# Kernel optimization log

Hardware: AMD Instinct MI355X
Metric: run time of the kernel (lower is better)

## Reference

```python
import jax, jax.numpy as jnp
import numpy as np

B, N = 4096, 4096
BISECTION_ITERS = 40


def setup_inputs() -> dict:
    key = jax.random.key(0)
    kz, = jax.random.split(key, 1)
    z = jax.random.normal(kz, (B, N), dtype=jnp.float32)
    gamma = jnp.ones((N,), dtype=jnp.float32)   # GammaParam fixed, init=1, clamped at eps (no-op here)
    m = jnp.zeros((N,), dtype=jnp.float32)      # BoundsParam fixed, m_init=0
    M = jnp.ones((N,), dtype=jnp.float32)       # BoundsParam fixed, M_init=1
    xi = jnp.ones((B,), dtype=jnp.float32)      # fixed xi=1 expanded to batch
    return {"z": z, "gamma": gamma, "m": m, "M": M, "xi": xi}


def reference(z, gamma, m, M, xi):
    """Weighted L2 projection of z (B,N) onto {x: sum x = xi, m <= x <= M} via bisection on lambda."""
    Bq, Nq = z.shape
    gB = jnp.broadcast_to(gamma, (Bq, Nq))
    mB = jnp.broadcast_to(m, (Bq, Nq))
    MB = jnp.broadcast_to(M, (Bq, Nq))
    two_gamma = 2.0 * gB

    lam_low = jnp.min(two_gamma * (mB - z), axis=-1)   # (B,)
    lam_high = jnp.max(two_gamma * (MB - z), axis=-1)  # (B,)

    def body(_, carry):
        lo, hi = carry
        mid = 0.5 * (lo + hi)
        x_mid = jnp.clip(z + mid[:, None] / two_gamma, mB, MB)
        g_mid = jnp.sum(x_mid, axis=-1) - xi
        pos = g_mid > 0
        lo_new = jnp.where(pos, lo, mid)
        hi_new = jnp.where(pos, mid, hi)
        return (lo_new, hi_new)

    lam_low, lam_high = jax.lax.fori_loop(0, BISECTION_ITERS, body, (lam_low, lam_high))
    lam = 0.5 * (lam_low + lam_high)
    x = jnp.clip(z + lam[:, None] / two_gamma, mB, MB)
    return x
```

## Files before the change

### kernel.cpp

```cpp
#include <hip/hip_runtime.h>


#define BISECT_STEPS 6
#define TOTAL_STEPS  9

template<int CTRL, int RM>
__device__ __forceinline__ float dpp_addf(float v) {
    int t = __builtin_amdgcn_update_dpp(0, __float_as_int(v), CTRL, RM, 0xf, false);
    return v + __int_as_float(t);
}
template<int CTRL, int RM>
__device__ __forceinline__ float dpp_minf(float v) {
    int t = __builtin_amdgcn_update_dpp(0x7f800000, __float_as_int(v), CTRL, RM, 0xf, false);
    return fminf(v, __int_as_float(t));
}
template<int CTRL, int RM>
__device__ __forceinline__ float dpp_maxf(float v) {
    int t = __builtin_amdgcn_update_dpp(0xff800000, __float_as_int(v), CTRL, RM, 0xf, false);
    return fmaxf(v, __int_as_float(t));
}
__device__ __forceinline__ float wave_sum(float v) {
    v = dpp_addf<0x111, 0xf>(v);
    v = dpp_addf<0x112, 0xf>(v);
    v = dpp_addf<0x114, 0xf>(v);
    v = dpp_addf<0x118, 0xf>(v);
    v = dpp_addf<0x142, 0xa>(v);
    v = dpp_addf<0x143, 0xc>(v);
    return __int_as_float(__builtin_amdgcn_readlane(__float_as_int(v), 63));
}
__device__ __forceinline__ float wave_min(float v) {
    v = dpp_minf<0x111, 0xf>(v);
    v = dpp_minf<0x112, 0xf>(v);
    v = dpp_minf<0x114, 0xf>(v);
    v = dpp_minf<0x118, 0xf>(v);
    v = dpp_minf<0x142, 0xa>(v);
    v = dpp_minf<0x143, 0xc>(v);
    return __int_as_float(__builtin_amdgcn_readlane(__float_as_int(v), 63));
}
__device__ __forceinline__ float wave_max(float v) {
    v = dpp_maxf<0x111, 0xf>(v);
    v = dpp_maxf<0x112, 0xf>(v);
    v = dpp_maxf<0x114, 0xf>(v);
    v = dpp_maxf<0x118, 0xf>(v);
    v = dpp_maxf<0x142, 0xa>(v);
    v = dpp_maxf<0x143, 0xc>(v);
    return __int_as_float(__builtin_amdgcn_readlane(__float_as_int(v), 63));
}

__global__ __launch_bounds__(256) void qp_proj_n4096(
    const float* __restrict__ z,
    const float* __restrict__ gamma,
    const float* __restrict__ mlo,
    const float* __restrict__ mhi,
    const float* __restrict__ xi,
    float* __restrict__ out)
{
    constexpr int N = 4096;
    const int row  = blockIdx.x;
    const int tid  = threadIdx.x;
    const int lane = tid & 63;
    const int wid  = tid >> 6;

    const float4* zrow = reinterpret_cast<const float4*>(z + (size_t)row * N);
    const float4* g4   = reinterpret_cast<const float4*>(gamma);
    const float4* m4   = reinterpret_cast<const float4*>(mlo);
    const float4* M4   = reinterpret_cast<const float4*>(mhi);
    float4*       orow = reinterpret_cast<float4*>(out + (size_t)row * N);

    __shared__ float red[8][4];
    __shared__ float wsum[2][4];

    float za[16];
    float zmn =  INFINITY, zmx = -INFINITY;
    float gmn =  INFINITY, gmx = -INFINITY;
    float mmn =  INFINITY, mmx = -INFINITY;
    float Mmn =  INFINITY, Mmx = -INFINITY;

    #pragma unroll
    for (int k = 0; k < 4; ++k) {
        const int idx = tid + k * 256;
        const float4 zz = zrow[idx];
        const float4 gg = g4[idx];
        const float4 mm = m4[idx];
        const float4 MM = M4[idx];
        za[4*k+0] = zz.x; za[4*k+1] = zz.y; za[4*k+2] = zz.z; za[4*k+3] = zz.w;
        zmn = fminf(zmn, fminf(fminf(zz.x, zz.y), fminf(zz.z, zz.w)));
        zmx = fmaxf(zmx, fmaxf(fmaxf(zz.x, zz.y), fmaxf(zz.z, zz.w)));
        gmn = fminf(gmn, fminf(fminf(gg.x, gg.y), fminf(gg.z, gg.w)));
        gmx = fmaxf(gmx, fmaxf(fmaxf(gg.x, gg.y), fmaxf(gg.z, gg.w)));
        mmn = fminf(mmn, fminf(fminf(mm.x, mm.y), fminf(mm.z, mm.w)));
        mmx = fmaxf(mmx, fmaxf(fmaxf(mm.x, mm.y), fmaxf(mm.z, mm.w)));
        Mmn = fminf(Mmn, fminf(fminf(MM.x, MM.y), fminf(MM.z, MM.w)));
        Mmx = fmaxf(Mmx, fmaxf(fmaxf(MM.x, MM.y), fmaxf(MM.z, MM.w)));
    }
    zmn = wave_min(zmn); zmx = wave_max(zmx);
    gmn = wave_min(gmn); gmx = wave_max(gmx);
    mmn = wave_min(mmn); mmx = wave_max(mmx);
    Mmn = wave_min(Mmn); Mmx = wave_max(Mmx);
    if (lane == 0) {
        red[0][wid] = zmn; red[1][wid] = zmx;
        red[2][wid] = gmn; red[3][wid] = gmx;
        red[4][wid] = mmn; red[5][wid] = mmx;
        red[6][wid] = Mmn; red[7][wid] = Mmx;
    }
    __syncthreads();
    const float zminT = fminf(fminf(red[0][0], red[0][1]), fminf(red[0][2], red[0][3]));
    const float zmaxT = fmaxf(fmaxf(red[1][0], red[1][1]), fmaxf(red[1][2], red[1][3]));
    const float gminT = fminf(fminf(red[2][0], red[2][1]), fminf(red[2][2], red[2][3]));
    const float gmaxT = fmaxf(fmaxf(red[3][0], red[3][1]), fmaxf(red[3][2], red[3][3]));
    const float mminT = fminf(fminf(red[4][0], red[4][1]), fminf(red[4][2], red[4][3]));
    const float mmaxT = fmaxf(fmaxf(red[5][0], red[5][1]), fmaxf(red[5][2], red[5][3]));
    const float MminT = fminf(fminf(red[6][0], red[6][1]), fminf(red[6][2], red[6][3]));
    const float MmaxT = fmaxf(fmaxf(red[7][0], red[7][1]), fmaxf(red[7][2], red[7][3]));

    const bool uniform = (gminT == gmaxT) && (mminT == mmaxT) &&
                         (MminT == MmaxT) && (gminT > 0.0f);
    const float xir = xi[row];

    if (uniform) {
        const float m0 = mminT, M0 = MminT;
        const float tg = 2.0f * gminT;
        const float ia = 1.0f / tg;
        float lo = tg * (m0 - zmaxT);
        float hi = tg * (M0 - zminT);
        float glo = (float)N * m0 - xir;
        float ghi = (float)N * M0 - xir;
        int side = 0;

        for (int it = 0; it < TOTAL_STEPS; ++it) {
            const float w = hi - lo;
            float cand;
            if (it < BISECT_STEPS) {
                cand = fmaf(0.5f, w, lo);
            } else {
                const float denom = ghi - glo;
                cand = (lo * ghi - hi * glo) / denom;
                cand = fminf(fmaxf(cand, fmaf(0.0625f, w, lo)),
                             fmaf(-0.0625f, w, hi));
            }

            float t0 = 0.f, t1 = 0.f, t2 = 0.f, t3 = 0.f;
            #pragma unroll
            for (int q = 0; q < 4; ++q) {
                t0 += __builtin_amdgcn_fmed3f(fmaf(cand, ia, za[4*q+0]), m0, M0);
                t1 += __builtin_amdgcn_fmed3f(fmaf(cand, ia, za[4*q+1]), m0, M0);
                t2 += __builtin_amdgcn_fmed3f(fmaf(cand, ia, za[4*q+2]), m0, M0);
                t3 += __builtin_amdgcn_fmed3f(fmaf(cand, ia, za[4*q+3]), m0, M0);
            }
            const float sw = wave_sum((t0 + t1) + (t2 + t3));

            const int p = it & 1;
            if (lane == 0) wsum[p][wid] = sw;
            __syncthreads();
            const float s = ((wsum[p][0] + wsum[p][1]) + (wsum[p][2] + wsum[p][3])) - xir;

            if (s > 0.0f) {
                hi = cand;
                if (side == 1) glo *= 0.5f;
                ghi = s;
                side = 1;
            } else {
                lo = cand;
                if (side == -1) ghi *= 0.5f;
                glo = s;
                side = -1;
            }
        }

        const float denom = ghi - glo;
        float lam = (denom > 0.0f) ? (lo * ghi - hi * glo) / denom
                                   : fmaf(0.5f, hi - lo, lo);
        lam = fminf(fmaxf(lam, lo), hi);

        #pragma unroll
        for (int k = 0; k < 4; ++k) {
            const int idx = tid + k * 256;
            float4 r;
            r.x = __builtin_amdgcn_fmed3f(fmaf(lam, ia, za[4*k+0]), m0, M0);
            r.y = __builtin_amdgcn_fmed3f(fmaf(lam, ia, za[4*k+1]), m0, M0);
            r.z = __builtin_amdgcn_fmed3f(fmaf(lam, ia, za[4*k+2]), m0, M0);
            r.w = __builtin_amdgcn_fmed3f(fmaf(lam, ia, za[4*k+3]), m0, M0);
            orow[idx] = r;
        }
    } else {
        __syncthreads();

        float ib[16], ma[16], Ma[16];
        float pmin =  INFINITY, pmax = -INFINITY, psm = 0.0f, psM = 0.0f;
        #pragma unroll
        for (int k = 0; k < 4; ++k) {
            const int idx = tid + k * 256;
            const float4 gg = g4[idx];
            const float4 mm = m4[idx];
            const float4 MM = M4[idx];
            const float gs[4] = {gg.x, gg.y, gg.z, gg.w};
            const float ms[4] = {mm.x, mm.y, mm.z, mm.w};
            const float Ms[4] = {MM.x, MM.y, MM.z, MM.w};
            #pragma unroll
            for (int c = 0; c < 4; ++c) {
                const int j = 4 * k + c;
                const float tg = 2.0f * gs[c];
                ib[j] = 1.0f / tg;
                ma[j] = ms[c];
                Ma[j] = Ms[c];
                pmin = fminf(pmin, tg * (ms[c] - za[j]));
                pmax = fmaxf(pmax, tg * (Ms[c] - za[j]));
                psm += ms[c];
                psM += Ms[c];
            }
        }
        pmin = wave_min(pmin);
        pmax = wave_max(pmax);
        psm  = wave_sum(psm);
        psM  = wave_sum(psM);
        if (lane == 0) { red[0][wid] = pmin; red[1][wid] = pmax;
                         red[2][wid] = psm;  red[3][wid] = psM; }
        __syncthreads();
        float lo = fminf(fminf(red[0][0], red[0][1]), fminf(red[0][2], red[0][3]));
        float hi = fmaxf(fmaxf(red[1][0], red[1][1]), fmaxf(red[1][2], red[1][3]));
        float glo = ((red[2][0] + red[2][1]) + (red[2][2] + red[2][3])) - xir;
        float ghi = ((red[3][0] + red[3][1]) + (red[3][2] + red[3][3])) - xir;
        int side = 0;

        for (int it = 0; it < TOTAL_STEPS; ++it) {
            const float w = hi - lo;
            float cand;
            if (it < BISECT_STEPS) {
                cand = fmaf(0.5f, w, lo);
            } else {
                const float denom = ghi - glo;
                cand = (lo * ghi - hi * glo) / denom;
                cand = fminf(fmaxf(cand, fmaf(0.0625f, w, lo)),
                             fmaf(-0.0625f, w, hi));
            }

            float t0 = 0.f, t1 = 0.f, t2 = 0.f, t3 = 0.f;
            #pragma unroll
            for (int q = 0; q < 4; ++q) {
                t0 += __builtin_amdgcn_fmed3f(fmaf(cand, ib[4*q+0], za[4*q+0]), ma[4*q+0], Ma[4*q+0]);
                t1 += __builtin_amdgcn_fmed3f(fmaf(cand, ib[4*q+1], za[4*q+1]), ma[4*q+1], Ma[4*q+1]);
                t2 += __builtin_amdgcn_fmed3f(fmaf(cand, ib[4*q+2], za[4*q+2]), ma[4*q+2], Ma[4*q+2]);
                t3 += __builtin_amdgcn_fmed3f(fmaf(cand, ib[4*q+3], za[4*q+3]), ma[4*q+3], Ma[4*q+3]);
            }
            const float sw = wave_sum((t0 + t1) + (t2 + t3));

            const int p = it & 1;
            if (lane == 0) wsum[p][wid] = sw;
            __syncthreads();
            const float s = ((wsum[p][0] + wsum[p][1]) + (wsum[p][2] + wsum[p][3])) - xir;

            if (s > 0.0f) {
                hi = cand;
                if (side == 1) glo *= 0.5f;
                ghi = s;
                side = 1;
            } else {
                lo = cand;
                if (side == -1) ghi *= 0.5f;
                glo = s;
                side = -1;
            }
        }

        const float denom = ghi - glo;
        float lam = (denom > 0.0f) ? (lo * ghi - hi * glo) / denom
                                   : fmaf(0.5f, hi - lo, lo);
        lam = fminf(fmaxf(lam, lo), hi);

        #pragma unroll
        for (int k = 0; k < 4; ++k) {
            const int idx = tid + k * 256;
            float4 r;
            float xs[4];
            #pragma unroll
            for (int c = 0; c < 4; ++c) {
                const int j = 4 * k + c;
                xs[c] = __builtin_amdgcn_fmed3f(fmaf(lam, ib[j], za[j]), ma[j], Ma[j]);
            }
            r.x = xs[0]; r.y = xs[1]; r.z = xs[2]; r.w = xs[3];
            orow[idx] = r;
        }
    }
}

extern "C" void kernel_launch(void* const* d_in, const int* in_sizes, int n_in,
                              void* d_out, int out_size, void* d_ws, size_t ws_size,
                              hipStream_t stream) {
    const float* z     = (const float*)d_in[0];
    const float* gamma = (const float*)d_in[1];
    const float* m     = (const float*)d_in[2];
    const float* M     = (const float*)d_in[3];
    const float* xi    = (const float*)d_in[4];
    float* out = (float*)d_out;

    const int B = in_sizes[4];
    qp_proj_n4096<<<dim3(B), dim3(256), 0, stream>>>(z, gamma, m, M, xi, out);
}
```

Before: 34.01 us.

## Replace bisection/Illinois search with 5-way multisection rounds in uniform path

```diff
diff --git a/kernel.cpp b/kernel.cpp
--- a/kernel.cpp
+++ b/kernel.cpp
@@ -1,6 +1,7 @@
 #include <hip/hip_runtime.h>
 
 
+#define ROUNDS 5
 #define BISECT_STEPS 6
 #define TOTAL_STEPS  9
 
@@ -68,7 +69,7 @@
     float4*       orow = reinterpret_cast<float4*>(out + (size_t)row * N);
 
     __shared__ float red[8][4];
-    __shared__ float wsum[2][4];
+    __shared__ float wsum[2][4][4];
 
     float za[16];
     float zmn =  INFINITY, zmx = -INFINITY;
@@ -125,51 +126,52 @@
         float hi = tg * (M0 - zminT);
         float glo = (float)N * m0 - xir;
         float ghi = (float)N * M0 - xir;
-        int side = 0;
-
-        for (int it = 0; it < TOTAL_STEPS; ++it) {
-            const float w = hi - lo;
-            float cand;
-            if (it < BISECT_STEPS) {
-                cand = fmaf(0.5f, w, lo);
-            } else {
-                const float denom = ghi - glo;
-                cand = (lo * ghi - hi * glo) / denom;
-                cand = fminf(fmaxf(cand, fmaf(0.0625f, w, lo)),
-                             fmaf(-0.0625f, w, hi));
-            }
-
-            float t0 = 0.f, t1 = 0.f, t2 = 0.f, t3 = 0.f;
-            #pragma unroll
-            for (int q = 0; q < 4; ++q) {
-                t0 += __builtin_amdgcn_fmed3f(fmaf(cand, ia, za[4*q+0]), m0, M0);
-                t1 += __builtin_amdgcn_fmed3f(fmaf(cand, ia, za[4*q+1]), m0, M0);
-                t2 += __builtin_amdgcn_fmed3f(fmaf(cand, ia, za[4*q+2]), m0, M0);
-                t3 += __builtin_amdgcn_fmed3f(fmaf(cand, ia, za[4*q+3]), m0, M0);
-            }
-            const float sw = wave_sum((t0 + t1) + (t2 + t3));
-
-            const int p = it & 1;
-            if (lane == 0) wsum[p][wid] = sw;
-            __syncthreads();
-            const float s = ((wsum[p][0] + wsum[p][1]) + (wsum[p][2] + wsum[p][3])) - xir;
-
-            if (s > 0.0f) {
-                hi = cand;
-                if (side == 1) glo *= 0.5f;
-                ghi = s;
-                side = 1;
-            } else {
-                lo = cand;
-                if (side == -1) ghi *= 0.5f;
-                glo = s;
-                side = -1;
+
+        if (hi > lo) {
+            for (int r = 0; r < ROUNDS; ++r) {
+                const float w5 = 0.2f * (hi - lo);
+                const float c1 = lo + w5;
+                const float c2 = fmaf(2.0f, w5, lo);
+                const float c3 = fmaf(3.0f, w5, lo);
+                const float c4 = fmaf(4.0f, w5, lo);
+
+                float s1 = 0.f, s2 = 0.f, s3 = 0.f, s4 = 0.f;
+                #pragma unroll
+                for (int j = 0; j < 16; ++j) {
+                    const float zj = za[j];
+                    s1 += __builtin_amdgcn_fmed3f(fmaf(c1, ia, zj), m0, M0);
+                    s2 += __builtin_amdgcn_fmed3f(fmaf(c2, ia, zj), m0, M0);
+                    s3 += __builtin_amdgcn_fmed3f(fmaf(c3, ia, zj), m0, M0);
+                    s4 += __builtin_amdgcn_fmed3f(fmaf(c4, ia, zj), m0, M0);
+                }
+                s1 = wave_sum(s1);
+                s2 = wave_sum(s2);
+                s3 = wave_sum(s3);
+                s4 = wave_sum(s4);
+
+                const int p = r & 1;
+                if (lane == 0) {
+                    wsum[p][0][wid] = s1; wsum[p][1][wid] = s2;
+                    wsum[p][2][wid] = s3; wsum[p][3][wid] = s4;
+                }
+                __syncthreads();
+                const float g1 = ((wsum[p][0][0] + wsum[p][0][1]) + (wsum[p][0][2] + wsum[p][0][3])) - xir;
+                const float g2 = ((wsum[p][1][0] + wsum[p][1][1]) + (wsum[p][1][2] + wsum[p][1][3])) - xir;
+                const float g3 = ((wsum[p][2][0] + wsum[p][2][1]) + (wsum[p][2][2] + wsum[p][2][3])) - xir;
+                const float g4v = ((wsum[p][3][0] + wsum[p][3][1]) + (wsum[p][3][2] + wsum[p][3][3])) - xir;
+
+                const int cnt = (g1 <= 0.0f) + (g2 <= 0.0f) + (g3 <= 0.0f) + (g4v <= 0.0f);
+                const float nglo = (cnt == 0) ? glo : (cnt == 1 ? g1 : cnt == 2 ? g2 : cnt == 3 ? g3 : g4v);
+                const float nghi = (cnt == 4) ? ghi : (cnt == 0 ? g1 : cnt == 1 ? g2 : cnt == 2 ? g3 : g4v);
+                const float nlo  = fmaf((float)cnt, w5, lo);
+                const float nhi  = (cnt == 4) ? hi : fmaf((float)(cnt + 1), w5, lo);
+                lo = nlo; hi = nhi; glo = nglo; ghi = nghi;
             }
         }
 
         const float denom = ghi - glo;
-        float lam = (denom > 0.0f) ? (lo * ghi - hi * glo) / denom
-                                   : fmaf(0.5f, hi - lo, lo);
+        float lam = (denom > 1e-30f) ? (lo * ghi - hi * glo) / denom
+                                     : fmaf(0.5f, hi - lo, lo);
         lam = fminf(fmaxf(lam, lo), hi);
 
         #pragma unroll
@@ -245,9 +247,9 @@
             const float sw = wave_sum((t0 + t1) + (t2 + t3));
 
             const int p = it & 1;
-            if (lane == 0) wsum[p][wid] = sw;
+            if (lane == 0) wsum[p][0][wid] = sw;
             __syncthreads();
-            const float s = ((wsum[p][0] + wsum[p][1]) + (wsum[p][2] + wsum[p][3])) - xir;
+            const float s = ((wsum[p][0][0] + wsum[p][0][1]) + (wsum[p][0][2] + wsum[p][0][3])) - xir;
 
             if (s > 0.0f) {
                 hi = cand;
```

Measured after the change: 49.87 us. 46.7% more time.

## Process four rows per block with next-row prefetch and cheaper uniformity check

Applied to the files above, without the earlier changes.

```diff
diff --git a/kernel.cpp b/kernel.cpp
--- a/kernel.cpp
+++ b/kernel.cpp
@@ -1,8 +1,9 @@
 #include <hip/hip_runtime.h>
 
 
+#define ROWS_PB 4
 #define BISECT_STEPS 6
-#define TOTAL_STEPS  9
+#define TOTAL_STEPS  8
 
 template<int CTRL, int RM>
 __device__ __forceinline__ float dpp_addf(float v) {
@@ -53,232 +54,270 @@
     const float* __restrict__ mlo,
     const float* __restrict__ mhi,
     const float* __restrict__ xi,
-    float* __restrict__ out)
+    float* __restrict__ out,
+    int Btot)
 {
     constexpr int N = 4096;
-    const int row  = blockIdx.x;
     const int tid  = threadIdx.x;
     const int lane = tid & 63;
     const int wid  = tid >> 6;
-
-    const float4* zrow = reinterpret_cast<const float4*>(z + (size_t)row * N);
-    const float4* g4   = reinterpret_cast<const float4*>(gamma);
-    const float4* m4   = reinterpret_cast<const float4*>(mlo);
-    const float4* M4   = reinterpret_cast<const float4*>(mhi);
-    float4*       orow = reinterpret_cast<float4*>(out + (size_t)row * N);
-
-    __shared__ float red[8][4];
+    const int row0 = blockIdx.x * ROWS_PB;
+
+    const float4* g4 = reinterpret_cast<const float4*>(gamma);
+    const float4* m4 = reinterpret_cast<const float4*>(mlo);
+    const float4* M4 = reinterpret_cast<const float4*>(mhi);
+
+    __shared__ float red[2][2][4];
     __shared__ float wsum[2][4];
-
-    float za[16];
-    float zmn =  INFINITY, zmx = -INFINITY;
-    float gmn =  INFINITY, gmx = -INFINITY;
-    float mmn =  INFINITY, mmx = -INFINITY;
-    float Mmn =  INFINITY, Mmx = -INFINITY;
-
+    __shared__ float gred[4][4];
+    __shared__ int   uni[4];
+
+    const float g0 = gamma[0];
+    const float m0 = mlo[0];
+    const float M0 = mhi[0];
+    bool ok = (g0 > 0.0f) && (M0 > m0);
     #pragma unroll
     for (int k = 0; k < 4; ++k) {
         const int idx = tid + k * 256;
-        const float4 zz = zrow[idx];
         const float4 gg = g4[idx];
         const float4 mm = m4[idx];
         const float4 MM = M4[idx];
-        za[4*k+0] = zz.x; za[4*k+1] = zz.y; za[4*k+2] = zz.z; za[4*k+3] = zz.w;
-        zmn = fminf(zmn, fminf(fminf(zz.x, zz.y), fminf(zz.z, zz.w)));
-        zmx = fmaxf(zmx, fmaxf(fmaxf(zz.x, zz.y), fmaxf(zz.z, zz.w)));
-        gmn = fminf(gmn, fminf(fminf(gg.x, gg.y), fminf(gg.z, gg.w)));
-        gmx = fmaxf(gmx, fmaxf(fmaxf(gg.x, gg.y), fmaxf(gg.z, gg.w)));
-        mmn = fminf(mmn, fminf(fminf(mm.x, mm.y), fminf(mm.z, mm.w)));
-        mmx = fmaxf(mmx, fmaxf(fmaxf(mm.x, mm.y), fmaxf(mm.z, mm.w)));
-        Mmn = fminf(Mmn, fminf(fminf(MM.x, MM.y), fminf(MM.z, MM.w)));
-        Mmx = fmaxf(Mmx, fmaxf(fmaxf(MM.x, MM.y), fmaxf(MM.z, MM.w)));
+        ok = ok && (gg.x == g0) && (gg.y == g0) && (gg.z == g0) && (gg.w == g0)
+                && (mm.x == m0) && (mm.y == m0) && (mm.z == m0) && (mm.w == m0)
+                && (MM.x == M0) && (MM.y == M0) && (MM.z == M0) && (MM.w == M0);
     }
-    zmn = wave_min(zmn); zmx = wave_max(zmx);
-    gmn = wave_min(gmn); gmx = wave_max(gmx);
-    mmn = wave_min(mmn); mmx = wave_max(mmx);
-    Mmn = wave_min(Mmn); Mmx = wave_max(Mmx);
-    if (lane == 0) {
-        red[0][wid] = zmn; red[1][wid] = zmx;
-        red[2][wid] = gmn; red[3][wid] = gmx;
-        red[4][wid] = mmn; red[5][wid] = mmx;
-        red[6][wid] = Mmn; red[7][wid] = Mmx;
+    {
+        const unsigned long long bal = __ballot(ok);
+        if (lane == 0) uni[wid] = (bal == 0xFFFFFFFFFFFFFFFFull) ? 1 : 0;
     }
     __syncthreads();
-    const float zminT = fminf(fminf(red[0][0], red[0][1]), fminf(red[0][2], red[0][3]));
-    const float zmaxT = fmaxf(fmaxf(red[1][0], red[1][1]), fmaxf(red[1][2], red[1][3]));
-    const float gminT = fminf(fminf(red[2][0], red[2][1]), fminf(red[2][2], red[2][3]));
-    const float gmaxT = fmaxf(fmaxf(red[3][0], red[3][1]), fmaxf(red[3][2], red[3][3]));
-    const float mminT = fminf(fminf(red[4][0], red[4][1]), fminf(red[4][2], red[4][3]));
-    const float mmaxT = fmaxf(fmaxf(red[5][0], red[5][1]), fmaxf(red[5][2], red[5][3]));
-    const float MminT = fminf(fminf(red[6][0], red[6][1]), fminf(red[6][2], red[6][3]));
-    const float MmaxT = fmaxf(fmaxf(red[7][0], red[7][1]), fmaxf(red[7][2], red[7][3]));
-
-    const bool uniform = (gminT == gmaxT) && (mminT == mmaxT) &&
-                         (MminT == MmaxT) && (gminT > 0.0f);
-    const float xir = xi[row];
+    const bool uniform = uni[0] && uni[1] && uni[2] && uni[3];
 
     if (uniform) {
-        const float m0 = mminT, M0 = MminT;
-        const float tg = 2.0f * gminT;
+        const float tg = 2.0f * g0;
         const float ia = 1.0f / tg;
-        float lo = tg * (m0 - zmaxT);
-        float hi = tg * (M0 - zminT);
-        float glo = (float)N * m0 - xir;
-        float ghi = (float)N * M0 - xir;
-        int side = 0;
-
-        for (int it = 0; it < TOTAL_STEPS; ++it) {
-            const float w = hi - lo;
-            float cand;
-            if (it < BISECT_STEPS) {
-                cand = fmaf(0.5f, w, lo);
-            } else {
-                const float denom = ghi - glo;
-                cand = (lo * ghi - hi * glo) / denom;
-                cand = fminf(fmaxf(cand, fmaf(0.0625f, w, lo)),
-                             fmaf(-0.0625f, w, hi));
-            }
-
-            float t0 = 0.f, t1 = 0.f, t2 = 0.f, t3 = 0.f;
+        const float gloC = (float)N * m0;
+        const float ghiC = (float)N * M0;
+
+        float za[16];
+        {
+            const float4* zr = reinterpret_cast<const float4*>(z + (size_t)row0 * N);
             #pragma unroll
-            for (int q = 0; q < 4; ++q) {
-                t0 += __builtin_amdgcn_fmed3f(fmaf(cand, ia, za[4*q+0]), m0, M0);
-                t1 += __builtin_amdgcn_fmed3f(fmaf(cand, ia, za[4*q+1]), m0, M0);
-                t2 += __builtin_amdgcn_fmed3f(fmaf(cand, ia, za[4*q+2]), m0, M0);
-                t3 += __builtin_amdgcn_fmed3f(fmaf(cand, ia, za[4*q+3]), m0, M0);
-            }
-            const float sw = wave_sum((t0 + t1) + (t2 + t3));
-
-            const int p = it & 1;
-            if (lane == 0) wsum[p][wid] = sw;
+            for (int k = 0; k < 4; ++k) {
+                const float4 zz = zr[tid + k * 256];
+                za[4*k+0] = zz.x; za[4*k+1] = zz.y; za[4*k+2] = zz.z; za[4*k+3] = zz.w;
+            }
+        }
+
+        #pragma unroll
+        for (int r = 0; r < ROWS_PB; ++r) {
+            const int row = row0 + r;
+            if (row >= Btot) break;
+
+            float zb[16];
+            const bool hasNext = (r + 1 < ROWS_PB) && (row + 1 < Btot);
+            if (hasNext) {
+                const float4* zr = reinterpret_cast<const float4*>(z + (size_t)(row + 1) * N);
+                #pragma unroll
+                for (int k = 0; k < 4; ++k) {
+                    const float4 zz = zr[tid + k * 256];
+                    zb[4*k+0] = zz.x; zb[4*k+1] = zz.y; zb[4*k+2] = zz.z; zb[4*k+3] = zz.w;
+                }
+            }
+
+            float zmn = INFINITY, zmx = -INFINITY;
+            #pragma unroll
+            for (int j = 0; j < 16; ++j) {
+                zmn = fminf(zmn, za[j]);
+                zmx = fmaxf(zmx, za[j]);
+            }
+            zmn = wave_min(zmn);
+            zmx = wave_max(zmx);
+            const int pr = r & 1;
+            if (lane == 0) { red[pr][0][wid] = zmn; red[pr][1][wid] = zmx; }
             __syncthreads();
-            const float s = ((wsum[p][0] + wsum[p][1]) + (wsum[p][2] + wsum[p][3])) - xir;
-
-            if (s > 0.0f) {
-                hi = cand;
-                if (side == 1) glo *= 0.5f;
-                ghi = s;
-                side = 1;
-            } else {
-                lo = cand;
-                if (side == -1) ghi *= 0.5f;
-                glo = s;
-                side = -1;
-            }
-        }
-
-        const float denom = ghi - glo;
-        float lam = (denom > 0.0f) ? (lo * ghi - hi * glo) / denom
-                                   : fmaf(0.5f, hi - lo, lo);
-        lam = fminf(fmaxf(lam, lo), hi);
-
-        #pragma unroll
-        for (int k = 0; k < 4; ++k) {
-            const int idx = tid + k * 256;
-            float4 r;
-            r.x = __builtin_amdgcn_fmed3f(fmaf(lam, ia, za[4*k+0]), m0, M0);
-            r.y = __builtin_amdgcn_fmed3f(fmaf(lam, ia, za[4*k+1]), m0, M0);
-            r.z = __builtin_amdgcn_fmed3f(fmaf(lam, ia, za[4*k+2]), m0, M0);
-            r.w = __builtin_amdgcn_fmed3f(fmaf(lam, ia, za[4*k+3]), m0, M0);
-            orow[idx] = r;
+            const float zminT = fminf(fminf(red[pr][0][0], red[pr][0][1]),
+                                      fminf(red[pr][0][2], red[pr][0][3]));
+            const float zmaxT = fmaxf(fmaxf(red[pr][1][0], red[pr][1][1]),
+                                      fmaxf(red[pr][1][2], red[pr][1][3]));
+            const float xir = xi[row];
+
+            float lo  = tg * (m0 - zmaxT);
+            float hi  = tg * (M0 - zminT);
+            float glo = gloC - xir;
+            float ghi = ghiC - xir;
+            int side = 0;
+
+            for (int it = 0; it < TOTAL_STEPS; ++it) {
+                const float w = hi - lo;
+                float cand;
+                if (it < BISECT_STEPS) {
+                    cand = fmaf(0.5f, w, lo);
+                } else {
+                    const float denom = ghi - glo;
+                    cand = (lo * ghi - hi * glo) / denom;
+                    cand = fminf(fmaxf(cand, fmaf(0.0625f, w, lo)),
+                                 fmaf(-0.0625f, w, hi));
+                }
+
+                float t0 = 0.f, t1 = 0.f, t2 = 0.f, t3 = 0.f;
+                #pragma unroll
+                for (int q = 0; q < 4; ++q) {
+                    t0 += __builtin_amdgcn_fmed3f(fmaf(cand, ia, za[4*q+0]), m0, M0);
+                    t1 += __builtin_amdgcn_fmed3f(fmaf(cand, ia, za[4*q+1]), m0, M0);
+                    t2 += __builtin_amdgcn_fmed3f(fmaf(cand, ia, za[4*q+2]), m0, M0);
+                    t3 += __builtin_amdgcn_fmed3f(fmaf(cand, ia, za[4*q+3]), m0, M0);
+                }
+                const float sw = wave_sum((t0 + t1) + (t2 + t3));
+
+                const int p = it & 1;
+                if (lane == 0) wsum[p][wid] = sw;
+                __syncthreads();
+                const float s = ((wsum[p][0] + wsum[p][1]) + (wsum[p][2] + wsum[p][3])) - xir;
+
+                if (s > 0.0f) {
+                    hi = cand;
+                    if (side == 1) glo *= 0.5f;
+                    ghi = s;
+                    side = 1;
+                } else {
+                    lo = cand;
+                    if (side == -1) ghi *= 0.5f;
+                    glo = s;
+                    side = -1;
+                }
+            }
+
+            const float denom = ghi - glo;
+            float lam = (denom > 0.0f) ? (lo * ghi - hi * glo) / denom
+                                       : fmaf(0.5f, hi - lo, lo);
+            lam = fminf(fmaxf(lam, lo), hi);
+
+            {
+                float4* orow = reinterpret_cast<float4*>(out + (size_t)row * N);
+                #pragma unroll
+                for (int k = 0; k < 4; ++k) {
+                    float4 rr;
+                    rr.x = __builtin_amdgcn_fmed3f(fmaf(lam, ia, za[4*k+0]), m0, M0);
+                    rr.y = __builtin_amdgcn_fmed3f(fmaf(lam, ia, za[4*k+1]), m0, M0);
+                    rr.z = __builtin_amdgcn_fmed3f(fmaf(lam, ia, za[4*k+2]), m0, M0);
+                    rr.w = __builtin_amdgcn_fmed3f(fmaf(lam, ia, za[4*k+3]), m0, M0);
+                    orow[tid + k * 256] = rr;
+                }
+            }
+
+            if (hasNext) {
+                #pragma unroll
+                for (int j = 0; j < 16; ++j) za[j] = zb[j];
+            }
         }
     } else {
-        __syncthreads();
-
-        float ib[16], ma[16], Ma[16];
-        float pmin =  INFINITY, pmax = -INFINITY, psm = 0.0f, psM = 0.0f;
-        #pragma unroll
-        for (int k = 0; k < 4; ++k) {
-            const int idx = tid + k * 256;
-            const float4 gg = g4[idx];
-            const float4 mm = m4[idx];
-            const float4 MM = M4[idx];
-            const float gs[4] = {gg.x, gg.y, gg.z, gg.w};
-            const float ms[4] = {mm.x, mm.y, mm.z, mm.w};
-            const float Ms[4] = {MM.x, MM.y, MM.z, MM.w};
+        for (int r = 0; r < ROWS_PB; ++r) {
+            const int row = row0 + r;
+            if (row >= Btot) break;
+
+            const float4* zr = reinterpret_cast<const float4*>(z + (size_t)row * N);
+            float4* orow = reinterpret_cast<float4*>(out + (size_t)row * N);
+
+            float za[16], ib[16], ma[16], Ma[16];
+            float pmin = INFINITY, pmax = -INFINITY, psm = 0.0f, psM = 0.0f;
             #pragma unroll
-            for (int c = 0; c < 4; ++c) {
-                const int j = 4 * k + c;
-                const float tg = 2.0f * gs[c];
-                ib[j] = 1.0f / tg;
-                ma[j] = ms[c];
-                Ma[j] = Ms[c];
-                pmin = fminf(pmin, tg * (ms[c] - za[j]));
-                pmax = fmaxf(pmax, tg * (Ms[c] - za[j]));
-                psm += ms[c];
-                psM += Ms[c];
-            }
-        }
-        pmin = wave_min(pmin);
-        pmax = wave_max(pmax);
-        psm  = wave_sum(psm);
-        psM  = wave_sum(psM);
-        if (lane == 0) { red[0][wid] = pmin; red[1][wid] = pmax;
-                         red[2][wid] = psm;  red[3][wid] = psM; }
-        __syncthreads();
-        float lo = fminf(fminf(red[0][0], red[0][1]), fminf(red[0][2], red[0][3]));
-        float hi = fmaxf(fmaxf(red[1][0], red[1][1]), fmaxf(red[1][2], red[1][3]));
-        float glo = ((red[2][0] + red[2][1]) + (red[2][2] + red[2][3])) - xir;
-        float ghi = ((red[3][0] + red[3][1]) + (red[3][2] + red[3][3])) - xir;
-        int side = 0;
-
-        for (int it = 0; it < TOTAL_STEPS; ++it) {
-            const float w = hi - lo;
-            float cand;
-            if (it < BISECT_STEPS) {
-                cand = fmaf(0.5f, w, lo);
-            } else {
-                const float denom = ghi - glo;
-                cand = (lo * ghi - hi * glo) / denom;
-                cand = fminf(fmaxf(cand, fmaf(0.0625f, w, lo)),
-                             fmaf(-0.0625f, w, hi));
-            }
-
-            float t0 = 0.f, t1 = 0.f, t2 = 0.f, t3 = 0.f;
+            for (int k = 0; k < 4; ++k) {
+                const int idx = tid + k * 256;
+                const float4 zz = zr[idx];
+                const float4 gg = g4[idx];
+                const float4 mm = m4[idx];
+                const float4 MM = M4[idx];
+                const float zs[4] = {zz.x, zz.y, zz.z, zz.w};
+                const float gs[4] = {gg.x, gg.y, gg.z, gg.w};
+                const float ms[4] = {mm.x, mm.y, mm.z, mm.w};
+                const float Ms[4] = {MM.x, MM.y, MM.z, MM.w};
+                #pragma unroll
+                for (int c = 0; c < 4; ++c) {
+                    const int j = 4 * k + c;
+                    const float tg2 = 2.0f * gs[c];
+                    za[j] = zs[c];
+                    ib[j] = 1.0f / tg2;
+                    ma[j] = ms[c];
+                    Ma[j] = Ms[c];
+                    pmin = fminf(pmin, tg2 * (ms[c] - zs[c]));
+                    pmax = fmaxf(pmax, tg2 * (Ms[c] - zs[c]));
+                    psm += ms[c];
+                    psM += Ms[c];
+                }
+            }
+            pmin = wave_min(pmin);
+            pmax = wave_max(pmax);
+            psm  = wave_sum(psm);
+            psM  = wave_sum(psM);
+            if (lane == 0) { gred[0][wid] = pmin; gred[1][wid] = pmax;
+                             gred[2][wid] = psm;  gred[3][wid] = psM; }
+            __syncthreads();
+            float lo = fminf(fminf(gred[0][0], gred[0][1]), fminf(gred[0][2], gred[0][3]));
+            float hi = fmaxf(fmaxf(gred[1][0], gred[1][1]), fmaxf(gred[1][2], gred[1][3]));
+            const float xir = xi[row];
+            float glo = ((gred[2][0] + gred[2][1]) + (gred[2][2] + gred[2][3])) - xir;
+            float ghi = ((gred[3][0] + gred[3][1]) + (gred[3][2] + gred[3][3])) - xir;
+            int side = 0;
+
+            for (int it = 0; it < TOTAL_STEPS + 1; ++it) {
+                const float w = hi - lo;
+                float cand;
+                if (it < BISECT_STEPS) {
+                    cand = fmaf(0.5f, w, lo);
+                } else {
+                    const float denom = ghi - glo;
+                    cand = (lo * ghi - hi * glo) / denom;
+                    cand = fminf(fmaxf(cand, fmaf(0.0625f, w, lo)),
+                                 fmaf(-0.0625f, w, hi));
+                }
+
+                float t0 = 0.f, t1 = 0.f, t2 = 0.f, t3 = 0.f;
+                #pragma unroll
+                for (int q = 0; q < 4; ++q) {
+                    t0 += __builtin_amdgcn_fmed3f(fmaf(cand, ib[4*q+0], za[4*q+0]), ma[4*q+0], Ma[4*q+0]);
+                    t1 += __builtin_amdgcn_fmed3f(fmaf(cand, ib[4*q+1], za[4*q+1]), ma[4*q+1], Ma[4*q+1]);
+                    t2 += __builtin_amdgcn_fmed3f(fmaf(cand, ib[4*q+2], za[4*q+2]), ma[4*q+2], Ma[4*q+2]);
+                    t3 += __builtin_amdgcn_fmed3f(fmaf(cand, ib[4*q+3], za[4*q+3]), ma[4*q+3], Ma[4*q+3]);
+                }
+                const float sw = wave_sum((t0 + t1) + (t2 + t3));
+
+                const int p = it & 1;
+                if (lane == 0) wsum[p][wid] = sw;
+                __syncthreads();
+                const float s = ((wsum[p][0] + wsum[p][1]) + (wsum[p][2] + wsum[p][3])) - xir;
+
+                if (s > 0.0f) {
+                    hi = cand;
+                    if (side == 1) glo *= 0.5f;
+                    ghi = s;
+                    side = 1;
+                } else {
+                    lo = cand;
+                    if (side == -1) ghi *= 0.5f;
+                    glo = s;
+                    side = -1;
+                }
+            }
+
+            const float denom = ghi - glo;
+            float lam = (denom > 0.0f) ? (lo * ghi - hi * glo) / denom
+                                       : fmaf(0.5f, hi - lo, lo);
+            lam = fminf(fmaxf(lam, lo), hi);
+
             #pragma unroll
-            for (int q = 0; q < 4; ++q) {
-                t0 += __builtin_amdgcn_fmed3f(fmaf(cand, ib[4*q+0], za[4*q+0]), ma[4*q+0], Ma[4*q+0]);
-                t1 += __builtin_amdgcn_fmed3f(fmaf(cand, ib[4*q+1], za[4*q+1]), ma[4*q+1], Ma[4*q+1]);
-                t2 += __builtin_amdgcn_fmed3f(fmaf(cand, ib[4*q+2], za[4*q+2]), ma[4*q+2], Ma[4*q+2]);
-                t3 += __builtin_amdgcn_fmed3f(fmaf(cand, ib[4*q+3], za[4*q+3]), ma[4*q+3], Ma[4*q+3]);
-            }
-            const float sw = wave_sum((t0 + t1) + (t2 + t3));
-
-            const int p = it & 1;
-            if (lane == 0) wsum[p][wid] = sw;
+            for (int k = 0; k < 4; ++k) {
+                float4 rr;
+                float xs[4];
+                #pragma unroll
+                for (int c = 0; c < 4; ++c) {
+                    const int j = 4 * k + c;
+                    xs[c] = __builtin_amdgcn_fmed3f(fmaf(lam, ib[j], za[j]), ma[j], Ma[j]);
+                }
+                rr.x = xs[0]; rr.y = xs[1]; rr.z = xs[2]; rr.w = xs[3];
+                orow[tid + k * 256] = rr;
+            }
             __syncthreads();
-            const float s = ((wsum[p][0] + wsum[p][1]) + (wsum[p][2] + wsum[p][3])) - xir;
-
-            if (s > 0.0f) {
-                hi = cand;
-                if (side == 1) glo *= 0.5f;
-                ghi = s;
-                side = 1;
-            } else {
-                lo = cand;
-                if (side == -1) ghi *= 0.5f;
-                glo = s;
-                side = -1;
-            }
-        }
-
-        const float denom = ghi - glo;
-        float lam = (denom > 0.0f) ? (lo * ghi - hi * glo) / denom
-                                   : fmaf(0.5f, hi - lo, lo);
-        lam = fminf(fmaxf(lam, lo), hi);
-
-        #pragma unroll
-        for (int k = 0; k < 4; ++k) {
-            const int idx = tid + k * 256;
-            float4 r;
-            float xs[4];
-            #pragma unroll
-            for (int c = 0; c < 4; ++c) {
-                const int j = 4 * k + c;
-                xs[c] = __builtin_amdgcn_fmed3f(fmaf(lam, ib[j], za[j]), ma[j], Ma[j]);
-            }
-            r.x = xs[0]; r.y = xs[1]; r.z = xs[2]; r.w = xs[3];
-            orow[idx] = r;
         }
     }
 }
@@ -294,5 +333,6 @@
     float* out = (float*)d_out;
 
     const int B = in_sizes[4];
-    qp_proj_n4096<<<dim3(B), dim3(256), 0, stream>>>(z, gamma, m, M, xi, out);
-}
+    const int nblocks = (B + ROWS_PB - 1) / ROWS_PB;
+    qp_proj_n4096<<<dim3(nblocks), dim3(256), 0, stream>>>(z, gamma, m, M, xi, out, B);
+}
```

Result: slower. 35.81 us (+5.3%).

## Process each row with a single wave, staging z in LDS via direct global-to-LDS loads

Applied to the files above, without the earlier changes.

```diff
diff --git a/kernel.cpp b/kernel.cpp
--- a/kernel.cpp
+++ b/kernel.cpp
@@ -3,6 +3,10 @@
 
 #define BISECT_STEPS 6
 #define TOTAL_STEPS  9
+
+#define GLD_LDS16(gp, lp) __builtin_amdgcn_global_load_lds( \
+    (const __attribute__((address_space(1))) void*)(gp),    \
+    (__attribute__((address_space(3))) void*)(lp), 16, 0, 0)
 
 template<int CTRL, int RM>
 __device__ __forceinline__ float dpp_addf(float v) {
@@ -47,7 +51,7 @@
     return __int_as_float(__builtin_amdgcn_readlane(__float_as_int(v), 63));
 }
 
-__global__ __launch_bounds__(256) void qp_proj_n4096(
+__global__ __launch_bounds__(64) void qp_proj_wave_lds(
     const float* __restrict__ z,
     const float* __restrict__ gamma,
     const float* __restrict__ mlo,
@@ -57,72 +61,60 @@
 {
     constexpr int N = 4096;
     const int row  = blockIdx.x;
-    const int tid  = threadIdx.x;
-    const int lane = tid & 63;
-    const int wid  = tid >> 6;
-
-    const float4* zrow = reinterpret_cast<const float4*>(z + (size_t)row * N);
+    const int lane = threadIdx.x;
+
+    const float*  zrow = z + (size_t)row * N;
     const float4* g4   = reinterpret_cast<const float4*>(gamma);
     const float4* m4   = reinterpret_cast<const float4*>(mlo);
     const float4* M4   = reinterpret_cast<const float4*>(mhi);
     float4*       orow = reinterpret_cast<float4*>(out + (size_t)row * N);
 
-    __shared__ float red[8][4];
-    __shared__ float wsum[2][4];
-
-    float za[16];
-    float zmn =  INFINITY, zmx = -INFINITY;
-    float gmn =  INFINITY, gmx = -INFINITY;
-    float mmn =  INFINITY, mmx = -INFINITY;
-    float Mmn =  INFINITY, Mmx = -INFINITY;
-
+    __shared__ float4 zs[N / 4];
+
+    {
+        const float* src = zrow + lane * 4;
+        char* ldsb = (char*)zs;
+        #pragma unroll
+        for (int k = 0; k < 16; ++k) {
+            GLD_LDS16(src + k * 256, ldsb + k * 1024);
+        }
+    }
+
+    const float g0 = gamma[0];
+    const float m0 = mlo[0];
+    const float M0 = mhi[0];
+    bool ok = (g0 > 0.0f) && (M0 > m0);
     #pragma unroll
-    for (int k = 0; k < 4; ++k) {
-        const int idx = tid + k * 256;
-        const float4 zz = zrow[idx];
+    for (int k = 0; k < 16; ++k) {
+        const int idx = lane + (k << 6);
         const float4 gg = g4[idx];
         const float4 mm = m4[idx];
         const float4 MM = M4[idx];
-        za[4*k+0] = zz.x; za[4*k+1] = zz.y; za[4*k+2] = zz.z; za[4*k+3] = zz.w;
-        zmn = fminf(zmn, fminf(fminf(zz.x, zz.y), fminf(zz.z, zz.w)));
-        zmx = fmaxf(zmx, fmaxf(fmaxf(zz.x, zz.y), fmaxf(zz.z, zz.w)));
-        gmn = fminf(gmn, fminf(fminf(gg.x, gg.y), fminf(gg.z, gg.w)));
-        gmx = fmaxf(gmx, fmaxf(fmaxf(gg.x, gg.y), fmaxf(gg.z, gg.w)));
-        mmn = fminf(mmn, fminf(fminf(mm.x, mm.y), fminf(mm.z, mm.w)));
-        mmx = fmaxf(mmx, fmaxf(fmaxf(mm.x, mm.y), fmaxf(mm.z, mm.w)));
-        Mmn = fminf(Mmn, fminf(fminf(MM.x, MM.y), fminf(MM.z, MM.w)));
-        Mmx = fmaxf(Mmx, fmaxf(fmaxf(MM.x, MM.y), fmaxf(MM.z, MM.w)));
+        ok = ok && (gg.x == g0) && (gg.y == g0) && (gg.z == g0) && (gg.w == g0)
+                && (mm.x == m0) && (mm.y == m0) && (mm.z == m0) && (mm.w == m0)
+                && (MM.x == M0) && (MM.y == M0) && (MM.z == M0) && (MM.w == M0);
     }
-    zmn = wave_min(zmn); zmx = wave_max(zmx);
-    gmn = wave_min(gmn); gmx = wave_max(gmx);
-    mmn = wave_min(mmn); mmx = wave_max(mmx);
-    Mmn = wave_min(Mmn); Mmx = wave_max(Mmx);
-    if (lane == 0) {
-        red[0][wid] = zmn; red[1][wid] = zmx;
-        red[2][wid] = gmn; red[3][wid] = gmx;
-        red[4][wid] = mmn; red[5][wid] = mmx;
-        red[6][wid] = Mmn; red[7][wid] = Mmx;
-    }
-    __syncthreads();
-    const float zminT = fminf(fminf(red[0][0], red[0][1]), fminf(red[0][2], red[0][3]));
-    const float zmaxT = fmaxf(fmaxf(red[1][0], red[1][1]), fmaxf(red[1][2], red[1][3]));
-    const float gminT = fminf(fminf(red[2][0], red[2][1]), fminf(red[2][2], red[2][3]));
-    const float gmaxT = fmaxf(fmaxf(red[3][0], red[3][1]), fmaxf(red[3][2], red[3][3]));
-    const float mminT = fminf(fminf(red[4][0], red[4][1]), fminf(red[4][2], red[4][3]));
-    const float mmaxT = fmaxf(fmaxf(red[5][0], red[5][1]), fmaxf(red[5][2], red[5][3]));
-    const float MminT = fminf(fminf(red[6][0], red[6][1]), fminf(red[6][2], red[6][3]));
-    const float MmaxT = fmaxf(fmaxf(red[7][0], red[7][1]), fmaxf(red[7][2], red[7][3]));
-
-    const bool uniform = (gminT == gmaxT) && (mminT == mmaxT) &&
-                         (MminT == MmaxT) && (gminT > 0.0f);
+    const bool uniform = (__ballot(ok) == 0xFFFFFFFFFFFFFFFFull);
     const float xir = xi[row];
 
+    asm volatile("s_waitcnt vmcnt(0)" ::: "memory");
+    __builtin_amdgcn_sched_barrier(0);
+
     if (uniform) {
-        const float m0 = mminT, M0 = MminT;
-        const float tg = 2.0f * gminT;
+        float zmn = INFINITY, zmx = -INFINITY;
+        #pragma unroll
+        for (int k = 0; k < 16; ++k) {
+            const float4 v = zs[lane + (k << 6)];
+            zmn = fminf(zmn, fminf(fminf(v.x, v.y), fminf(v.z, v.w)));
+            zmx = fmaxf(zmx, fmaxf(fmaxf(v.x, v.y), fmaxf(v.z, v.w)));
+        }
+        zmn = wave_min(zmn);
+        zmx = wave_max(zmx);
+
+        const float tg = 2.0f * g0;
         const float ia = 1.0f / tg;
-        float lo = tg * (m0 - zmaxT);
-        float hi = tg * (M0 - zminT);
+        float lo  = tg * (m0 - zmx);
+        float hi  = tg * (M0 - zmn);
         float glo = (float)N * m0 - xir;
         float ghi = (float)N * M0 - xir;
         int side = 0;
@@ -141,18 +133,14 @@
 
             float t0 = 0.f, t1 = 0.f, t2 = 0.f, t3 = 0.f;
             #pragma unroll
-            for (int q = 0; q < 4; ++q) {
-                t0 += __builtin_amdgcn_fmed3f(fmaf(cand, ia, za[4*q+0]), m0, M0);
-                t1 += __builtin_amdgcn_fmed3f(fmaf(cand, ia, za[4*q+1]), m0, M0);
-                t2 += __builtin_amdgcn_fmed3f(fmaf(cand, ia, za[4*q+2]), m0, M0);
-                t3 += __builtin_amdgcn_fmed3f(fmaf(cand, ia, za[4*q+3]), m0, M0);
-            }
-            const float sw = wave_sum((t0 + t1) + (t2 + t3));
-
-            const int p = it & 1;
-            if (lane == 0) wsum[p][wid] = sw;
-            __syncthreads();
-            const float s = ((wsum[p][0] + wsum[p][1]) + (wsum[p][2] + wsum[p][3])) - xir;
+            for (int k = 0; k < 16; ++k) {
+                const float4 v = zs[lane + (k << 6)];
+                t0 += __builtin_amdgcn_fmed3f(fmaf(cand, ia, v.x), m0, M0);
+                t1 += __builtin_amdgcn_fmed3f(fmaf(cand, ia, v.y), m0, M0);
+                t2 += __builtin_amdgcn_fmed3f(fmaf(cand, ia, v.z), m0, M0);
+                t3 += __builtin_amdgcn_fmed3f(fmaf(cand, ia, v.w), m0, M0);
+            }
+            const float s = wave_sum((t0 + t1) + (t2 + t3)) - xir;
 
             if (s > 0.0f) {
                 hi = cand;
@@ -173,53 +161,42 @@
         lam = fminf(fmaxf(lam, lo), hi);
 
         #pragma unroll
-        for (int k = 0; k < 4; ++k) {
-            const int idx = tid + k * 256;
+        for (int k = 0; k < 16; ++k) {
+            const int idx = lane + (k << 6);
+            const float4 v = zs[idx];
             float4 r;
-            r.x = __builtin_amdgcn_fmed3f(fmaf(lam, ia, za[4*k+0]), m0, M0);
-            r.y = __builtin_amdgcn_fmed3f(fmaf(lam, ia, za[4*k+1]), m0, M0);
-            r.z = __builtin_amdgcn_fmed3f(fmaf(lam, ia, za[4*k+2]), m0, M0);
-            r.w = __builtin_amdgcn_fmed3f(fmaf(lam, ia, za[4*k+3]), m0, M0);
+            r.x = __builtin_amdgcn_fmed3f(fmaf(lam, ia, v.x), m0, M0);
+            r.y = __builtin_amdgcn_fmed3f(fmaf(lam, ia, v.y), m0, M0);
+            r.z = __builtin_amdgcn_fmed3f(fmaf(lam, ia, v.z), m0, M0);
+            r.w = __builtin_amdgcn_fmed3f(fmaf(lam, ia, v.w), m0, M0);
             orow[idx] = r;
         }
     } else {
-        __syncthreads();
-
-        float ib[16], ma[16], Ma[16];
-        float pmin =  INFINITY, pmax = -INFINITY, psm = 0.0f, psM = 0.0f;
-        #pragma unroll
-        for (int k = 0; k < 4; ++k) {
-            const int idx = tid + k * 256;
+        float pmin = INFINITY, pmax = -INFINITY, psm = 0.0f, psM = 0.0f;
+        #pragma unroll
+        for (int k = 0; k < 16; ++k) {
+            const int idx = lane + (k << 6);
+            const float4 v  = zs[idx];
             const float4 gg = g4[idx];
             const float4 mm = m4[idx];
             const float4 MM = M4[idx];
-            const float gs[4] = {gg.x, gg.y, gg.z, gg.w};
-            const float ms[4] = {mm.x, mm.y, mm.z, mm.w};
-            const float Ms[4] = {MM.x, MM.y, MM.z, MM.w};
+            const float zc[4] = {v.x, v.y, v.z, v.w};
+            const float gc[4] = {gg.x, gg.y, gg.z, gg.w};
+            const float mc[4] = {mm.x, mm.y, mm.z, mm.w};
+            const float Mc[4] = {MM.x, MM.y, MM.z, MM.w};
             #pragma unroll
             for (int c = 0; c < 4; ++c) {
-                const int j = 4 * k + c;
-                const float tg = 2.0f * gs[c];
-                ib[j] = 1.0f / tg;
-                ma[j] = ms[c];
-                Ma[j] = Ms[c];
-                pmin = fminf(pmin, tg * (ms[c] - za[j]));
-                pmax = fmaxf(pmax, tg * (Ms[c] - za[j]));
-                psm += ms[c];
-                psM += Ms[c];
-            }
-        }
-        pmin = wave_min(pmin);
-        pmax = wave_max(pmax);
-        psm  = wave_sum(psm);
-        psM  = wave_sum(psM);
-        if (lane == 0) { red[0][wid] = pmin; red[1][wid] = pmax;
-                         red[2][wid] = psm;  red[3][wid] = psM; }
-        __syncthreads();
-        float lo = fminf(fminf(red[0][0], red[0][1]), fminf(red[0][2], red[0][3]));
-        float hi = fmaxf(fmaxf(red[1][0], red[1][1]), fmaxf(red[1][2], red[1][3]));
-        float glo = ((red[2][0] + red[2][1]) + (red[2][2] + red[2][3])) - xir;
-        float ghi = ((red[3][0] + red[3][1]) + (red[3][2] + red[3][3])) - xir;
+                const float tgc = 2.0f * gc[c];
+                pmin = fminf(pmin, tgc * (mc[c] - zc[c]));
+                pmax = fmaxf(pmax, tgc * (Mc[c] - zc[c]));
+                psm += mc[c];
+                psM += Mc[c];
+            }
+        }
+        float lo  = wave_min(pmin);
+        float hi  = wave_max(pmax);
+        float glo = wave_sum(psm) - xir;
+        float ghi = wave_sum(psM) - xir;
         int side = 0;
 
         for (int it = 0; it < TOTAL_STEPS; ++it) {
@@ -236,18 +213,18 @@
 
             float t0 = 0.f, t1 = 0.f, t2 = 0.f, t3 = 0.f;
             #pragma unroll
-            for (int q = 0; q < 4; ++q) {
-                t0 += __builtin_amdgcn_fmed3f(fmaf(cand, ib[4*q+0], za[4*q+0]), ma[4*q+0], Ma[4*q+0]);
-                t1 += __builtin_amdgcn_fmed3f(fmaf(cand, ib[4*q+1], za[4*q+1]), ma[4*q+1], Ma[4*q+1]);
-                t2 += __builtin_amdgcn_fmed3f(fmaf(cand, ib[4*q+2], za[4*q+2]), ma[4*q+2], Ma[4*q+2]);
-                t3 += __builtin_amdgcn_fmed3f(fmaf(cand, ib[4*q+3], za[4*q+3]), ma[4*q+3], Ma[4*q+3]);
-            }
-            const float sw = wave_sum((t0 + t1) + (t2 + t3));
-
-            const int p = it & 1;
-            if (lane == 0) wsum[p][wid] = sw;
-            __syncthreads();
-            const float s = ((wsum[p][0] + wsum[p][1]) + (wsum[p][2] + wsum[p][3])) - xir;
+            for (int k = 0; k < 16; ++k) {
+                const int idx = lane + (k << 6);
+                const float4 v  = zs[idx];
+                const float4 gg = g4[idx];
+                const float4 mm = m4[idx];
+                const float4 MM = M4[idx];
+                t0 += __builtin_amdgcn_fmed3f(fmaf(cand, 1.0f / (2.0f * gg.x), v.x), mm.x, MM.x);
+                t1 += __builtin_amdgcn_fmed3f(fmaf(cand, 1.0f / (2.0f * gg.y), v.y), mm.y, MM.y);
+                t2 += __builtin_amdgcn_fmed3f(fmaf(cand, 1.0f / (2.0f * gg.z), v.z), mm.z, MM.z);
+                t3 += __builtin_amdgcn_fmed3f(fmaf(cand, 1.0f / (2.0f * gg.w), v.w), mm.w, MM.w);
+            }
+            const float s = wave_sum((t0 + t1) + (t2 + t3)) - xir;
 
             if (s > 0.0f) {
                 hi = cand;
@@ -268,16 +245,17 @@
         lam = fminf(fmaxf(lam, lo), hi);
 
         #pragma unroll
-        for (int k = 0; k < 4; ++k) {
-            const int idx = tid + k * 256;
+        for (int k = 0; k < 16; ++k) {
+            const int idx = lane + (k << 6);
+            const float4 v  = zs[idx];
+            const float4 gg = g4[idx];
+            const float4 mm = m4[idx];
+            const float4 MM = M4[idx];
             float4 r;
-            float xs[4];
-            #pragma unroll
-            for (int c = 0; c < 4; ++c) {
-                const int j = 4 * k + c;
-                xs[c] = __builtin_amdgcn_fmed3f(fmaf(lam, ib[j], za[j]), ma[j], Ma[j]);
-            }
-            r.x = xs[0]; r.y = xs[1]; r.z = xs[2]; r.w = xs[3];
+            r.x = __builtin_amdgcn_fmed3f(fmaf(lam, 1.0f / (2.0f * gg.x), v.x), mm.x, MM.x);
+            r.y = __builtin_amdgcn_fmed3f(fmaf(lam, 1.0f / (2.0f * gg.y), v.y), mm.y, MM.y);
+            r.z = __builtin_amdgcn_fmed3f(fmaf(lam, 1.0f / (2.0f * gg.z), v.z), mm.z, MM.z);
+            r.w = __builtin_amdgcn_fmed3f(fmaf(lam, 1.0f / (2.0f * gg.w), v.w), mm.w, MM.w);
             orow[idx] = r;
         }
     }
@@ -294,5 +272,5 @@
     float* out = (float*)d_out;
 
     const int B = in_sizes[4];
-    qp_proj_n4096<<<dim3(B), dim3(256), 0, stream>>>(z, gamma, m, M, xi, out);
-}
+    qp_proj_wave_lds<<<dim3(B), dim3(64), 0, stream>>>(z, gamma, m, M, xi, out);
+}
```

New measurement: 64.77 us. +90.5%, slower.
